# Kernel tuning notes

Hardware: AMD Instinct MI355X
Metric: run time of the kernel (lower is better)

Reference implementation:

```python
import jax, jax.numpy as jnp
import numpy as np


def setup_inputs() -> dict:
    key = jax.random.key(0)
    k1, k2, k3 = jax.random.split(key, 3)
    B, L, IN, MEM = 64, 512, 512, 1024
    u = jax.random.normal(k1, (B, L, IN), dtype=jnp.float32)
    # torch Linear weights: [out_features, in_features], kaiming-uniform-ish scale
    W_im = jax.random.normal(k2, (3 * MEM, IN), dtype=jnp.float32) / np.sqrt(IN)
    W_mm = jax.random.normal(k3, (2 * MEM, MEM), dtype=jnp.float32) / np.sqrt(MEM)
    return {"u": u, "W_im": W_im, "W_mm": W_mm}


def reference(u, W_im, W_mm):
    B, L, _ = u.shape
    mem = W_mm.shape[1]
    # Input projection has no sequential dependency: batch it over all timesteps.
    in_emb = jnp.einsum('bli,ji->blj', u, W_im)  # (B, L, 3*mem)

    def step(h, e):
        i_a, i_c, i_o = jnp.split(e, 3, axis=-1)
        m = jnp.einsum('bm,jm->bj', h, W_mm)     # (B, 2*mem)
        m_a, m_c = jnp.split(m, 2, axis=-1)
        a = 1.0 + jnp.tanh(i_a + m_a)
        c = jax.nn.sigmoid(i_c + m_c)
        h_next = c * h + (1.0 - c) * jnp.tanh(i_o + a * h)
        return h_next, h_next

    h0 = jnp.zeros((B, mem), dtype=u.dtype)
    _, hs = jax.lax.scan(step, h0, jnp.swapaxes(in_emb, 0, 1))  # hs: (L, B, mem)
    h_seq = jnp.swapaxes(hs, 0, 1)                               # (B, L, mem)
    return h_seq, h_seq[:, -1:, :]
```

## Files before the change

### kernel.cpp

```cpp
#include <hip/hip_runtime.h>


typedef __attribute__((ext_vector_type(8))) short short8;
typedef __attribute__((ext_vector_type(4))) float floatx4;

#define WS_HBUF_OFF 402653184UL

__device__ __forceinline__ unsigned short f2bf(float x) {
  unsigned u = __float_as_uint(x);
  unsigned r = (u + 0x7fffu + ((u >> 16) & 1u)) >> 16;
  return (unsigned short)r;
}
__device__ __forceinline__ float bf2f(unsigned short h) {
  return __uint_as_float(((unsigned)h) << 16);
}
__device__ __forceinline__ float fast_tanh(float x) {
  x = fminf(15.0f, fmaxf(-15.0f, x));
  const float e = __expf(2.0f * x);
  return (e - 1.0f) / (e + 1.0f);
}
__device__ __forceinline__ float fast_sigmoid(float x) {
  return 1.0f / (1.0f + __expf(-x));
}

__global__ void __launch_bounds__(256, 2) gemm_in_proj(
    const float* __restrict__ U, const float* __restrict__ Wim,
    float* __restrict__ E)
{
  __shared__ unsigned short Ah[128][40], Al[128][40], Bh[128][40], Bl[128][40];
  const int tid = threadIdx.x;
  const int rbase = blockIdx.x * 128;
  const int nbase = blockIdx.y * 128;
  const int wave = tid >> 6, lane = tid & 63;
  const int wm = wave & 1, wn = wave >> 1;
  const int q = lane >> 4, ln = lane & 15;

  floatx4 acc[4][4];
#pragma unroll
  for (int mt = 0; mt < 4; ++mt)
#pragma unroll
    for (int nt = 0; nt < 4; ++nt)
      acc[mt][nt] = (floatx4){0.f, 0.f, 0.f, 0.f};

  for (int kc = 0; kc < 16; ++kc) {
    __syncthreads();
#pragma unroll
    for (int i = tid; i < 1024; i += 256) {
      const int row = i >> 3, c4 = (i & 7) << 2;
      const float4 va = *(const float4*)(U + (rbase + row) * 512 + kc * 32 + c4);
      const unsigned short a0 = f2bf(va.x), a1 = f2bf(va.y), a2 = f2bf(va.z), a3 = f2bf(va.w);
      *(ushort4*)&Ah[row][c4] = make_ushort4(a0, a1, a2, a3);
      *(ushort4*)&Al[row][c4] = make_ushort4(f2bf(va.x - bf2f(a0)), f2bf(va.y - bf2f(a1)),
                                             f2bf(va.z - bf2f(a2)), f2bf(va.w - bf2f(a3)));
      const float4 vb = *(const float4*)(Wim + (nbase + row) * 512 + kc * 32 + c4);
      const unsigned short b0 = f2bf(vb.x), b1 = f2bf(vb.y), b2 = f2bf(vb.z), b3 = f2bf(vb.w);
      *(ushort4*)&Bh[row][c4] = make_ushort4(b0, b1, b2, b3);
      *(ushort4*)&Bl[row][c4] = make_ushort4(f2bf(vb.x - bf2f(b0)), f2bf(vb.y - bf2f(b1)),
                                             f2bf(vb.z - bf2f(b2)), f2bf(vb.w - bf2f(b3)));
    }
    __syncthreads();

    short8 ah[4], al[4], bh[4], bl2[4];
#pragma unroll
    for (int mt = 0; mt < 4; ++mt) {
      const int m = wm * 64 + mt * 16 + ln;
      ah[mt] = *(const short8*)&Ah[m][q * 8];
      al[mt] = *(const short8*)&Al[m][q * 8];
    }
#pragma unroll
    for (int nt = 0; nt < 4; ++nt) {
      const int n = wn * 64 + nt * 16 + ln;
      bh[nt]  = *(const short8*)&Bh[n][q * 8];
      bl2[nt] = *(const short8*)&Bl[n][q * 8];
    }
#pragma unroll
    for (int mt = 0; mt < 4; ++mt)
#pragma unroll
      for (int nt = 0; nt < 4; ++nt) {
        acc[mt][nt] = __builtin_amdgcn_mfma_f32_16x16x32_bf16(ah[mt], bh[nt],  acc[mt][nt], 0, 0, 0);
        acc[mt][nt] = __builtin_amdgcn_mfma_f32_16x16x32_bf16(al[mt], bh[nt],  acc[mt][nt], 0, 0, 0);
        acc[mt][nt] = __builtin_amdgcn_mfma_f32_16x16x32_bf16(ah[mt], bl2[nt], acc[mt][nt], 0, 0, 0);
      }
  }

#pragma unroll
  for (int mt = 0; mt < 4; ++mt)
#pragma unroll
    for (int nt = 0; nt < 4; ++nt)
#pragma unroll
      for (int r = 0; r < 4; ++r) {
        const int gm = rbase + wm * 64 + mt * 16 + q * 4 + r;
        const int gn = nbase + wn * 64 + nt * 16 + ln;
        E[gm * 3072 + gn] = acc[mt][nt][r];
      }
}

__global__ void __launch_bounds__(256, 1) rnn_scan(
    const float* __restrict__ E,
    const float* __restrict__ Wmm,
    unsigned* __restrict__ hbuf,
    float* __restrict__ out)
{
  __shared__ float part[2][4 * 16 * 33];

  const int tid = threadIdx.x;
  const int bg  = blockIdx.x >> 6;
  const int cg  = blockIdx.x & 63;
  const int b0  = bg << 4;
  const int j0  = cg << 4;

  const int kq = tid >> 6;
  const int lane = tid & 63;
  const int q = lane >> 4, ln = lane & 15;

  short8 wh[2][8], wl[2][8];
#pragma unroll
  for (int nt = 0; nt < 2; ++nt) {
    const int row = (nt ? 1024 + j0 + ln : j0 + ln);
    const float* wp = Wmm + row * 1024 + kq * 256 + q * 8;
#pragma unroll
    for (int ks = 0; ks < 8; ++ks) {
      const float4 f0 = *(const float4*)(wp + ks * 32);
      const float4 f1 = *(const float4*)(wp + ks * 32 + 4);
      float f[8] = {f0.x, f0.y, f0.z, f0.w, f1.x, f1.y, f1.z, f1.w};
      short8 h8, l8;
#pragma unroll
      for (int e = 0; e < 8; ++e) {
        const unsigned short hh = f2bf(f[e]);
        h8[e] = (short)hh;
        l8[e] = (short)f2bf(f[e] - bf2f(hh));
      }
      wh[nt][ks] = h8; wl[nt][ks] = l8;
    }
  }

  const int b_l = tid >> 4, jp = tid & 15;
  const int b = b0 + b_l, j = j0 + jp;

  float h_reg = 0.0f;
  const unsigned long long* hbuf64 = (const unsigned long long*)hbuf;
  const unsigned hbase64 = ((unsigned)(b0 + ln)) * 512 + (unsigned)kq * 128 + (unsigned)q * 4;
  const unsigned cano64  = ((unsigned)(b0 + ln)) * 512 + (unsigned)kq * 128 + (unsigned)ln * 8 + (unsigned)q * 2;

  int erow = (b * 512) * 3072 + j;
  float ia = E[erow], ic = E[erow + 1024], io = E[erow + 2048];

  for (int t = 0; t < 512; ++t) {
    const int cur = t & 1, nxt = cur ^ 1;
    const unsigned tg = (unsigned)t & 3u;

    {
      const unsigned long long* cp = hbuf64 + (unsigned)cur * 32768u + cano64;
      int spins = 0;
      for (;;) {
        const unsigned long long c = __hip_atomic_load(
            (unsigned long long*)cp, __ATOMIC_RELAXED, __HIP_MEMORY_SCOPE_SYSTEM);
        const unsigned ok = ((((unsigned)(c >> 16)) & 3u) == tg) &
                            ((((unsigned)(c >> 48)) & 3u) == tg);
        if (__all((int)ok)) break;
        if (++spins > 3000) break;
        __builtin_amdgcn_s_sleep(1);
      }
      __atomic_signal_fence(__ATOMIC_ACQUIRE);
    }

    const unsigned long long* hrow = hbuf64 + (unsigned)cur * 32768u + hbase64;

    floatx4 acc0, acc1;
    int vspins = 0;
    for (;;) {
      acc0 = (floatx4){0.f, 0.f, 0.f, 0.f};
      acc1 = (floatx4){0.f, 0.f, 0.f, 0.f};
      unsigned ok = 1u;
#pragma unroll
      for (int ks = 0; ks < 8; ++ks) {
        unsigned long long d0 = __hip_atomic_load((unsigned long long*)(hrow + ks * 16 + 0),
                                                  __ATOMIC_RELAXED, __HIP_MEMORY_SCOPE_SYSTEM);
        unsigned long long d1 = __hip_atomic_load((unsigned long long*)(hrow + ks * 16 + 1),
                                                  __ATOMIC_RELAXED, __HIP_MEMORY_SCOPE_SYSTEM);
        unsigned long long d2 = __hip_atomic_load((unsigned long long*)(hrow + ks * 16 + 2),
                                                  __ATOMIC_RELAXED, __HIP_MEMORY_SCOPE_SYSTEM);
        unsigned long long d3 = __hip_atomic_load((unsigned long long*)(hrow + ks * 16 + 3),
                                                  __ATOMIC_RELAXED, __HIP_MEMORY_SCOPE_SYSTEM);
        ok &= (((unsigned)(d0 >> 16) & 3u) == tg) & (((unsigned)(d0 >> 48) & 3u) == tg);
        ok &= (((unsigned)(d1 >> 16) & 3u) == tg) & (((unsigned)(d1 >> 48) & 3u) == tg);
        ok &= (((unsigned)(d2 >> 16) & 3u) == tg) & (((unsigned)(d2 >> 48) & 3u) == tg);
        ok &= (((unsigned)(d3 >> 16) & 3u) == tg) & (((unsigned)(d3 >> 48) & 3u) == tg);
        const unsigned pp[8] = {(unsigned)d0, (unsigned)(d0 >> 32),
                                (unsigned)d1, (unsigned)(d1 >> 32),
                                (unsigned)d2, (unsigned)(d2 >> 32),
                                (unsigned)d3, (unsigned)(d3 >> 32)};
        short8 ah, al;
#pragma unroll
        for (int e = 0; e < 8; ++e) {
          ah[e] = (short)(pp[e] & 0xffffu);
          al[e] = (short)(pp[e] >> 16);
        }
        acc0 = __builtin_amdgcn_mfma_f32_16x16x32_bf16(ah, wh[0][ks], acc0, 0, 0, 0);
        acc0 = __builtin_amdgcn_mfma_f32_16x16x32_bf16(al, wh[0][ks], acc0, 0, 0, 0);
        acc0 = __builtin_amdgcn_mfma_f32_16x16x32_bf16(ah, wl[0][ks], acc0, 0, 0, 0);
        acc1 = __builtin_amdgcn_mfma_f32_16x16x32_bf16(ah, wh[1][ks], acc1, 0, 0, 0);
        acc1 = __builtin_amdgcn_mfma_f32_16x16x32_bf16(al, wh[1][ks], acc1, 0, 0, 0);
        acc1 = __builtin_amdgcn_mfma_f32_16x16x32_bf16(ah, wl[1][ks], acc1, 0, 0, 0);
      }
      if (__all((int)ok)) break;
      if (++vspins > 1000) break;
      __builtin_amdgcn_s_sleep(1);
    }

#pragma unroll
    for (int r = 0; r < 4; ++r) {
      part[cur][(kq * 16 + q * 4 + r) * 33 + ln]      = acc0[r];
      part[cur][(kq * 16 + q * 4 + r) * 33 + 16 + ln] = acc1[r];
    }
    __syncthreads();

    const float m_a = part[cur][(0 * 16 + b_l) * 33 + jp]      + part[cur][(1 * 16 + b_l) * 33 + jp]
                    + part[cur][(2 * 16 + b_l) * 33 + jp]      + part[cur][(3 * 16 + b_l) * 33 + jp];
    const float m_c = part[cur][(0 * 16 + b_l) * 33 + 16 + jp] + part[cur][(1 * 16 + b_l) * 33 + 16 + jp]
                    + part[cur][(2 * 16 + b_l) * 33 + 16 + jp] + part[cur][(3 * 16 + b_l) * 33 + 16 + jp];

    const float av = 1.0f + fast_tanh(ia + m_a);
    const float cv = fast_sigmoid(ic + m_c);
    const float hn = cv * h_reg + (1.0f - cv) * fast_tanh(io + av * h_reg);
    h_reg = hn;

    const unsigned short hh = f2bf(hn);
    unsigned short hl = f2bf(hn - bf2f(hh));
    hl = (unsigned short)((hl & 0xFFFCu) | (unsigned)((t + 1) & 3));
    __hip_atomic_store(hbuf + (unsigned)nxt * 65536u + (unsigned)b * 1024u + (unsigned)j,
                       (unsigned)hh | ((unsigned)hl << 16),
                       __ATOMIC_RELAXED, __HIP_MEMORY_SCOPE_SYSTEM);

    __hip_atomic_store(out + (unsigned)(b * 512 + t) * 1024u + (unsigned)j, hn,
                       __ATOMIC_RELAXED, __HIP_MEMORY_SCOPE_SYSTEM);

    erow += 3072;
    if (t < 511) {
      ia = E[erow];
      ic = E[erow + 1024];
      io = E[erow + 2048];
    }
  }

  out[33554432 + b * 1024 + j] = h_reg;
}

extern "C" void kernel_launch(void* const* d_in, const int* in_sizes, int n_in,
                              void* d_out, int out_size, void* d_ws, size_t ws_size,
                              hipStream_t stream)
{
  const float* U   = (const float*)d_in[0];
  const float* Wim = (const float*)d_in[1];
  const float* Wmm = (const float*)d_in[2];
  float* out = (float*)d_out;
  char* ws = (char*)d_ws;

  float* E = (float*)ws;
  unsigned* hbuf = (unsigned*)(ws + WS_HBUF_OFF);

  hipMemsetAsync((void*)hbuf, 0, 524288, stream);

  gemm_in_proj<<<dim3(256, 24), dim3(256), 0, stream>>>(U, Wim, E);

  rnn_scan<<<dim3(256), dim3(256), 0, stream>>>(E, Wmm, hbuf, out);
}
```

Baseline: 3.586 ms.

## Use 1024-thread blocks that stage the shared h slab in LDS

The recurrent scan now runs as 64 blocks of 1024 threads, each covering 16 batches by 64 hidden columns, instead of 256 blocks of 256 threads. Each block loads its whole 16x1024 hidden-state slab from global memory once per step, checks the step tags, then splits the packed bf16 hi/lo pairs into LDS so all 16 waves read MFMA operands from shared memory. This removes the duplicated global reads and the spin-retry MFMA loop that each wave group used to run. In exchange each block waits on a larger slab and adds an extra __syncthreads per step, and far fewer CUs stay active, so per-step latency inside a block may rise.

```diff
diff --git a/kernel.cpp b/kernel.cpp
--- a/kernel.cpp
+++ b/kernel.cpp
@@ -95,28 +95,32 @@
       }
 }
 
-__global__ void __launch_bounds__(256, 1) rnn_scan(
+__global__ void __launch_bounds__(1024, 1) rnn_scan(
     const float* __restrict__ E,
     const float* __restrict__ Wmm,
     unsigned* __restrict__ hbuf,
     float* __restrict__ out)
 {
-  __shared__ float part[2][4 * 16 * 33];
+  __shared__ unsigned short hh[16][1032];
+  __shared__ unsigned short hl[16][1032];
+  __shared__ float part[4][16][132];
 
   const int tid = threadIdx.x;
-  const int bg  = blockIdx.x >> 6;
-  const int cg  = blockIdx.x & 63;
+  const int bg  = blockIdx.x >> 4;
+  const int cg  = blockIdx.x & 15;
   const int b0  = bg << 4;
-  const int j0  = cg << 4;
-
-  const int kq = tid >> 6;
+  const int J0  = cg << 6;
+
+  const int wid  = tid >> 6;
   const int lane = tid & 63;
+  const int kq = wid & 3;
+  const int ng = wid >> 2;
   const int q = lane >> 4, ln = lane & 15;
 
   short8 wh[2][8], wl[2][8];
 #pragma unroll
   for (int nt = 0; nt < 2; ++nt) {
-    const int row = (nt ? 1024 + j0 + ln : j0 + ln);
+    const int row = (nt ? 1024 : 0) + J0 + ng * 16 + ln;
     const float* wp = Wmm + row * 1024 + kq * 256 + q * 8;
 #pragma unroll
     for (int ks = 0; ks < 8; ++ks) {
@@ -126,21 +130,20 @@
       short8 h8, l8;
 #pragma unroll
       for (int e = 0; e < 8; ++e) {
-        const unsigned short hh = f2bf(f[e]);
-        h8[e] = (short)hh;
-        l8[e] = (short)f2bf(f[e] - bf2f(hh));
+        const unsigned short hhv = f2bf(f[e]);
+        h8[e] = (short)hhv;
+        l8[e] = (short)f2bf(f[e] - bf2f(hhv));
       }
       wh[nt][ks] = h8; wl[nt][ks] = l8;
     }
   }
 
-  const int b_l = tid >> 4, jp = tid & 15;
-  const int b = b0 + b_l, j = j0 + jp;
+  const int b_l = tid >> 6, jc = tid & 63;
+  const int b = b0 + b_l, j = J0 + jc;
 
   float h_reg = 0.0f;
   const unsigned long long* hbuf64 = (const unsigned long long*)hbuf;
-  const unsigned hbase64 = ((unsigned)(b0 + ln)) * 512 + (unsigned)kq * 128 + (unsigned)q * 4;
-  const unsigned cano64  = ((unsigned)(b0 + ln)) * 512 + (unsigned)kq * 128 + (unsigned)ln * 8 + (unsigned)q * 2;
+  const unsigned slab0 = (unsigned)b0 * 512u;
 
   int erow = (b * 512) * 3072 + j;
   float ia = E[erow], ic = E[erow + 1024], io = E[erow + 2048];
@@ -149,87 +152,81 @@
     const int cur = t & 1, nxt = cur ^ 1;
     const unsigned tg = (unsigned)t & 3u;
 
+    const unsigned long long* sp = hbuf64 + (unsigned)cur * 32768u + slab0;
+    unsigned long long d[8];
     {
-      const unsigned long long* cp = hbuf64 + (unsigned)cur * 32768u + cano64;
       int spins = 0;
       for (;;) {
-        const unsigned long long c = __hip_atomic_load(
-            (unsigned long long*)cp, __ATOMIC_RELAXED, __HIP_MEMORY_SCOPE_SYSTEM);
-        const unsigned ok = ((((unsigned)(c >> 16)) & 3u) == tg) &
-                            ((((unsigned)(c >> 48)) & 3u) == tg);
+        unsigned ok = 1u;
+#pragma unroll
+        for (int c = 0; c < 4; ++c) {
+          const unsigned idx = (unsigned)c * 2048u + (unsigned)tid * 2u;
+          d[2 * c]     = __hip_atomic_load(sp + idx,     __ATOMIC_RELAXED, __HIP_MEMORY_SCOPE_SYSTEM);
+          d[2 * c + 1] = __hip_atomic_load(sp + idx + 1, __ATOMIC_RELAXED, __HIP_MEMORY_SCOPE_SYSTEM);
+        }
+#pragma unroll
+        for (int c = 0; c < 8; ++c) {
+          ok &= (((unsigned)(d[c] >> 16) & 3u) == tg) &
+                (((unsigned)(d[c] >> 48) & 3u) == tg);
+        }
         if (__all((int)ok)) break;
         if (++spins > 3000) break;
         __builtin_amdgcn_s_sleep(1);
       }
       __atomic_signal_fence(__ATOMIC_ACQUIRE);
     }
-
-    const unsigned long long* hrow = hbuf64 + (unsigned)cur * 32768u + hbase64;
-
-    floatx4 acc0, acc1;
-    int vspins = 0;
-    for (;;) {
-      acc0 = (floatx4){0.f, 0.f, 0.f, 0.f};
-      acc1 = (floatx4){0.f, 0.f, 0.f, 0.f};
-      unsigned ok = 1u;
-#pragma unroll
-      for (int ks = 0; ks < 8; ++ks) {
-        unsigned long long d0 = __hip_atomic_load((unsigned long long*)(hrow + ks * 16 + 0),
-                                                  __ATOMIC_RELAXED, __HIP_MEMORY_SCOPE_SYSTEM);
-        unsigned long long d1 = __hip_atomic_load((unsigned long long*)(hrow + ks * 16 + 1),
-                                                  __ATOMIC_RELAXED, __HIP_MEMORY_SCOPE_SYSTEM);
-        unsigned long long d2 = __hip_atomic_load((unsigned long long*)(hrow + ks * 16 + 2),
-                                                  __ATOMIC_RELAXED, __HIP_MEMORY_SCOPE_SYSTEM);
-        unsigned long long d3 = __hip_atomic_load((unsigned long long*)(hrow + ks * 16 + 3),
-                                                  __ATOMIC_RELAXED, __HIP_MEMORY_SCOPE_SYSTEM);
-        ok &= (((unsigned)(d0 >> 16) & 3u) == tg) & (((unsigned)(d0 >> 48) & 3u) == tg);
-        ok &= (((unsigned)(d1 >> 16) & 3u) == tg) & (((unsigned)(d1 >> 48) & 3u) == tg);
-        ok &= (((unsigned)(d2 >> 16) & 3u) == tg) & (((unsigned)(d2 >> 48) & 3u) == tg);
-        ok &= (((unsigned)(d3 >> 16) & 3u) == tg) & (((unsigned)(d3 >> 48) & 3u) == tg);
-        const unsigned pp[8] = {(unsigned)d0, (unsigned)(d0 >> 32),
-                                (unsigned)d1, (unsigned)(d1 >> 32),
-                                (unsigned)d2, (unsigned)(d2 >> 32),
-                                (unsigned)d3, (unsigned)(d3 >> 32)};
-        short8 ah, al;
-#pragma unroll
-        for (int e = 0; e < 8; ++e) {
-          ah[e] = (short)(pp[e] & 0xffffu);
-          al[e] = (short)(pp[e] >> 16);
-        }
-        acc0 = __builtin_amdgcn_mfma_f32_16x16x32_bf16(ah, wh[0][ks], acc0, 0, 0, 0);
-        acc0 = __builtin_amdgcn_mfma_f32_16x16x32_bf16(al, wh[0][ks], acc0, 0, 0, 0);
-        acc0 = __builtin_amdgcn_mfma_f32_16x16x32_bf16(ah, wl[0][ks], acc0, 0, 0, 0);
-        acc1 = __builtin_amdgcn_mfma_f32_16x16x32_bf16(ah, wh[1][ks], acc1, 0, 0, 0);
-        acc1 = __builtin_amdgcn_mfma_f32_16x16x32_bf16(al, wh[1][ks], acc1, 0, 0, 0);
-        acc1 = __builtin_amdgcn_mfma_f32_16x16x32_bf16(ah, wl[1][ks], acc1, 0, 0, 0);
-      }
-      if (__all((int)ok)) break;
-      if (++vspins > 1000) break;
-      __builtin_amdgcn_s_sleep(1);
+#pragma unroll
+    for (int c = 0; c < 4; ++c) {
+      const unsigned idx = (unsigned)c * 2048u + (unsigned)tid * 2u;
+      const int bb = (int)(idx >> 9);
+      const int c0 = (int)((idx & 511u) << 1);
+      const unsigned w0 = (unsigned)d[2 * c],     w1 = (unsigned)(d[2 * c] >> 32);
+      const unsigned w2 = (unsigned)d[2 * c + 1], w3 = (unsigned)(d[2 * c + 1] >> 32);
+      *(ushort4*)&hh[bb][c0] = make_ushort4((unsigned short)(w0 & 0xffffu), (unsigned short)(w1 & 0xffffu),
+                                            (unsigned short)(w2 & 0xffffu), (unsigned short)(w3 & 0xffffu));
+      *(ushort4*)&hl[bb][c0] = make_ushort4((unsigned short)(w0 >> 16), (unsigned short)(w1 >> 16),
+                                            (unsigned short)(w2 >> 16), (unsigned short)(w3 >> 16));
+    }
+    __syncthreads();
+
+    floatx4 acc0 = (floatx4){0.f, 0.f, 0.f, 0.f};
+    floatx4 acc1 = (floatx4){0.f, 0.f, 0.f, 0.f};
+#pragma unroll
+    for (int ks = 0; ks < 8; ++ks) {
+      const int kb = kq * 256 + ks * 32 + q * 8;
+      const short8 ah = *(const short8*)&hh[ln][kb];
+      const short8 al = *(const short8*)&hl[ln][kb];
+      acc0 = __builtin_amdgcn_mfma_f32_16x16x32_bf16(ah, wh[0][ks], acc0, 0, 0, 0);
+      acc0 = __builtin_amdgcn_mfma_f32_16x16x32_bf16(al, wh[0][ks], acc0, 0, 0, 0);
+      acc0 = __builtin_amdgcn_mfma_f32_16x16x32_bf16(ah, wl[0][ks], acc0, 0, 0, 0);
+      acc1 = __builtin_amdgcn_mfma_f32_16x16x32_bf16(ah, wh[1][ks], acc1, 0, 0, 0);
+      acc1 = __builtin_amdgcn_mfma_f32_16x16x32_bf16(al, wh[1][ks], acc1, 0, 0, 0);
+      acc1 = __builtin_amdgcn_mfma_f32_16x16x32_bf16(ah, wl[1][ks], acc1, 0, 0, 0);
     }
 
 #pragma unroll
     for (int r = 0; r < 4; ++r) {
-      part[cur][(kq * 16 + q * 4 + r) * 33 + ln]      = acc0[r];
-      part[cur][(kq * 16 + q * 4 + r) * 33 + 16 + ln] = acc1[r];
-    }
-    __syncthreads();
-
-    const float m_a = part[cur][(0 * 16 + b_l) * 33 + jp]      + part[cur][(1 * 16 + b_l) * 33 + jp]
-                    + part[cur][(2 * 16 + b_l) * 33 + jp]      + part[cur][(3 * 16 + b_l) * 33 + jp];
-    const float m_c = part[cur][(0 * 16 + b_l) * 33 + 16 + jp] + part[cur][(1 * 16 + b_l) * 33 + 16 + jp]
-                    + part[cur][(2 * 16 + b_l) * 33 + 16 + jp] + part[cur][(3 * 16 + b_l) * 33 + 16 + jp];
+      part[kq][q * 4 + r][ng * 32 + ln]      = acc0[r];
+      part[kq][q * 4 + r][ng * 32 + 16 + ln] = acc1[r];
+    }
+    __syncthreads();
+
+    const int sa = (jc >> 4) * 32 + (jc & 15);
+    const float m_a = part[0][b_l][sa]      + part[1][b_l][sa]
+                    + part[2][b_l][sa]      + part[3][b_l][sa];
+    const float m_c = part[0][b_l][sa + 16] + part[1][b_l][sa + 16]
+                    + part[2][b_l][sa + 16] + part[3][b_l][sa + 16];
 
     const float av = 1.0f + fast_tanh(ia + m_a);
     const float cv = fast_sigmoid(ic + m_c);
     const float hn = cv * h_reg + (1.0f - cv) * fast_tanh(io + av * h_reg);
     h_reg = hn;
 
-    const unsigned short hh = f2bf(hn);
-    unsigned short hl = f2bf(hn - bf2f(hh));
-    hl = (unsigned short)((hl & 0xFFFCu) | (unsigned)((t + 1) & 3));
+    const unsigned short hhv = f2bf(hn);
+    unsigned short hlv = f2bf(hn - bf2f(hhv));
+    hlv = (unsigned short)((hlv & 0xFFFCu) | (unsigned)((t + 1) & 3));
     __hip_atomic_store(hbuf + (unsigned)nxt * 65536u + (unsigned)b * 1024u + (unsigned)j,
-                       (unsigned)hh | ((unsigned)hl << 16),
+                       (unsigned)hhv | ((unsigned)hlv << 16),
                        __ATOMIC_RELAXED, __HIP_MEMORY_SCOPE_SYSTEM);
 
     __hip_atomic_store(out + (unsigned)(b * 512 + t) * 1024u + (unsigned)j, hn,
@@ -263,5 +260,5 @@
 
   gemm_in_proj<<<dim3(256, 24), dim3(256), 0, stream>>>(U, Wim, E);
 
-  rnn_scan<<<dim3(256), dim3(256), 0, stream>>>(E, Wmm, hbuf, out);
-}
+  rnn_scan<<<dim3(64), dim3(1024), 0, stream>>>(E, Wmm, hbuf, out);
+}
```

Result: slower. 6.496 ms (+81.2%).
